# Kernel tuning notes

Measured on AMD Instinct MI355X. Metric: run time of the kernel, lower is better.

## Reference

```python
import jax, jax.numpy as jnp
import numpy as np

B, Q, C = 16, 3000, 1203


def setup_inputs() -> dict:
    key = jax.random.key(0)
    k1, k2, k3, k4 = jax.random.split(key, 4)
    pred_logits = jax.random.normal(k1, (B, Q, C), dtype=jnp.float32)
    pred_boxes = jax.random.uniform(k2, (B, Q, 4), dtype=jnp.float32)
    target_sizes = jax.random.randint(k3, (B, 2), 0, 1333, dtype=jnp.int64)
    class_present = jax.random.randint(k4, (B, C), 0, 2) > 0  # bool [B, C]
    return {
        "pred_logits": pred_logits,
        "pred_boxes": pred_boxes,
        "target_sizes": target_sizes,
        "class_present": class_present,
    }


def reference(pred_logits, pred_boxes, target_sizes, class_present):
    # prob[b,q,c] = sigmoid(logits); keep if prob >= 0.5 * max_q prob[b,:,c]
    # AND class c is in targets[b]['labels'] (class_present mask).
    del target_sizes  # only shape-asserted in the original forward
    prob = jax.nn.sigmoid(pred_logits)                      # [B,Q,C]
    top = jnp.max(prob, axis=1, keepdims=True)              # [B,1,C]
    keep = (prob >= 0.5 * top) & class_present[:, None, :]   # [B,Q,C] bool
    scores = jnp.where(keep, prob, jnp.zeros((), prob.dtype))  # masked scores
    box_keep = jnp.any(keep, axis=2)                        # [B,Q] query kept for some class
    boxes = pred_boxes * box_keep[..., None].astype(pred_boxes.dtype)  # [B,Q,4]
    return scores, keep, boxes
```

## Files before the change

kernel.cpp:

```cpp
#include <hip/hip_runtime.h>
#include <math.h>

#define NB 16
#define NQR 3000
#define NC 1203

typedef float f32x4 __attribute__((ext_vector_type(4)));

__device__ __forceinline__ int lane_proc(float x, float t,
                                         float* __restrict__ s,
                                         float* __restrict__ k) {
    float pf = __builtin_amdgcn_rcpf(1.0f + __expf(-x));
    bool kp;
    float sc;
    if (pf > t + 1e-5f) {
        kp = true;  sc = pf;
    } else if (pf < t - 1e-5f) {
        kp = false; sc = 0.0f;
    } else {
        float e32 = (float)exp(-(double)x);
        float p32 = 1.0f / (1.0f + e32);
        kp = (p32 >= t);
        sc = kp ? p32 : 0.0f;
    }
    *s = sc;
    *k = kp ? 1.0f : 0.0f;
    return kp ? 1 : 0;
}

__global__ void k_partial_max(const float* __restrict__ logits,
                              float* __restrict__ partial,
                              int qc) {
    int c = blockIdx.x * blockDim.x + threadIdx.x;
    int b = blockIdx.y;
    int z = blockIdx.z;
    if (c >= NC) return;
    int q0 = z * qc;
    int q1 = min(NQR, q0 + qc);
    float m = -INFINITY;
    const float* p = logits + ((size_t)(b * NQR + q0)) * NC + c;
    int q = q0;
    for (; q + 8 <= q1; q += 8) {
        float a0 = p[0];
        float a1 = p[NC];
        float a2 = p[2 * NC];
        float a3 = p[3 * NC];
        float a4 = p[4 * NC];
        float a5 = p[5 * NC];
        float a6 = p[6 * NC];
        float a7 = p[7 * NC];
        float m01 = fmaxf(a0, a1), m23 = fmaxf(a2, a3);
        float m45 = fmaxf(a4, a5), m67 = fmaxf(a6, a7);
        m = fmaxf(m, fmaxf(fmaxf(m01, m23), fmaxf(m45, m67)));
        p += 8 * NC;
    }
    for (; q < q1; ++q) {
        m = fmaxf(m, *p);
        p += NC;
    }
    partial[((size_t)z * NB + b) * NC + c] = m;
}

__global__ void k_thresh(const float* __restrict__ partial,
                         const int* __restrict__ cls_present,
                         float* __restrict__ thrf,
                         int nz) {
    int c = blockIdx.x * blockDim.x + threadIdx.x;
    int b = blockIdx.y;
    if (c >= NC) return;
    float m = -INFINITY;
    for (int z = 0; z < nz; ++z)
        m = fmaxf(m, partial[((size_t)z * NB + b) * NC + c]);
    float t;
    if (cls_present[b * NC + c]) {
        float e32  = (float)exp(-(double)m);
        float ptop = 1.0f / (1.0f + e32);
        t = 0.5f * ptop;
    } else {
        t = INFINITY;
    }
    thrf[(size_t)b * NC + c] = t;
}

__global__ __launch_bounds__(256) void k_main(const float* __restrict__ logits,
                                              const float* __restrict__ boxes,
                                              const float* __restrict__ thrf,
                                              float* __restrict__ scores,
                                              float* __restrict__ keep,
                                              float* __restrict__ boxes_out) {
    int wid  = threadIdx.x >> 6;
    int lane = threadIdx.x & 63;
    int row  = blockIdx.x * 4 + wid;
    int b    = row / NQR;

    const float* lrow = logits + (size_t)row * NC;
    const float* tf   = thrf + (size_t)b * NC;
    float* srow = scores + (size_t)row * NC;
    float* krow = keep + (size_t)row * NC;

    int head = row & 3;
    int any = 0;
    float sv, kv;

    f32x4 x[5];
    int cb[5];
    bool act[5];
#pragma unroll
    for (int i = 0; i < 5; ++i) {
        int v = lane + 64 * i;
        act[i] = (v < 300);
        cb[i] = head + 4 * v;
        if (act[i]) x[i] = *(const f32x4*)(lrow + cb[i]);
    }

    if (lane < head) {
        int c = lane;
        any |= lane_proc(lrow[c], tf[c], &sv, &kv);
        __builtin_nontemporal_store(sv, srow + c);
        __builtin_nontemporal_store(kv, krow + c);
    }

#pragma unroll
    for (int i = 0; i < 5; ++i) {
        if (act[i]) {
            int c = cb[i];
            f32x4 x4 = x[i];
            f32x4 s4, k4;
            float s0, s1, s2, s3, k0, k1, k2, k3;
            any |= lane_proc(x4.x, tf[c + 0], &s0, &k0);
            any |= lane_proc(x4.y, tf[c + 1], &s1, &k1);
            any |= lane_proc(x4.z, tf[c + 2], &s2, &k2);
            any |= lane_proc(x4.w, tf[c + 3], &s3, &k3);
            s4 = (f32x4){s0, s1, s2, s3};
            k4 = (f32x4){k0, k1, k2, k3};
            __builtin_nontemporal_store(s4, (f32x4*)(srow + c));
            __builtin_nontemporal_store(k4, (f32x4*)(krow + c));
        }
    }

    if (lane < 3 - head) {
        int c = head + 1200 + lane;
        any |= lane_proc(lrow[c], tf[c], &sv, &kv);
        __builtin_nontemporal_store(sv, srow + c);
        __builtin_nontemporal_store(kv, krow + c);
    }

    unsigned long long m = __ballot(any);
    if (lane == 0) {
        float mm = m ? 1.0f : 0.0f;
        f32x4 bx = *(const f32x4*)(boxes + (size_t)row * 4);
        f32x4 o = bx * mm;
        *(f32x4*)(boxes_out + (size_t)row * 4) = o;
    }
}

extern "C" void kernel_launch(void* const* d_in, const int* in_sizes, int n_in,
                              void* d_out, int out_size, void* d_ws, size_t ws_size,
                              hipStream_t stream) {
    const float* logits      = (const float*)d_in[0];
    const float* boxes       = (const float*)d_in[1];
    const int*   cls_present = (const int*)d_in[3];

    float* scores    = (float*)d_out;
    float* keep      = scores + (size_t)NB * NQR * NC;
    float* boxes_out = keep + (size_t)NB * NQR * NC;

    int nz = 25;
    while (nz > 1 && ((size_t)nz + 1) * NB * NC * sizeof(float) > ws_size)
        nz /= 2;
    float* partial = (float*)d_ws;
    float* thrf    = partial + (size_t)nz * NB * NC;
    int qc = (NQR + nz - 1) / nz;

    dim3 gmax((NC + 255) / 256, NB, nz);
    k_partial_max<<<gmax, 256, 0, stream>>>(logits, partial, qc);

    dim3 gthr((NC + 255) / 256, NB);
    k_thresh<<<gthr, 256, 0, stream>>>(partial, cls_present, thrf, nz);

    k_main<<<(NB * NQR) / 4, 256, 0, stream>>>(logits, boxes, thrf,
                                               scores, keep, boxes_out);
}
```

Before: 195.6 us.

## Split batch into chunks so main pass rereads logits from cache

The three-kernel pipeline now runs over three batch chunks (6, 5 and 5 images), so the max pass and the main pass touch a smaller slice of logits back to back. The intent is for that slice to still sit in the large last-level cache when k_main reads it again, instead of coming from HBM. The main kernel also swaps its up-front load of all five vectors for a one-ahead software prefetch, which lowers register pressure. The cost is more kernel launches and smaller grids per launch, which may hurt occupancy and add launch gaps.

```diff
diff --git a/kernel.cpp b/kernel.cpp
--- a/kernel.cpp
+++ b/kernel.cpp
@@ -30,9 +30,9 @@
 
 __global__ void k_partial_max(const float* __restrict__ logits,
                               float* __restrict__ partial,
-                              int qc) {
+                              int qc, int b0) {
     int c = blockIdx.x * blockDim.x + threadIdx.x;
-    int b = blockIdx.y;
+    int b = blockIdx.y + b0;
     int z = blockIdx.z;
     if (c >= NC) return;
     int q0 = z * qc;
@@ -64,9 +64,9 @@
 __global__ void k_thresh(const float* __restrict__ partial,
                          const int* __restrict__ cls_present,
                          float* __restrict__ thrf,
-                         int nz) {
+                         int nz, int b0) {
     int c = blockIdx.x * blockDim.x + threadIdx.x;
-    int b = blockIdx.y;
+    int b = blockIdx.y + b0;
     if (c >= NC) return;
     float m = -INFINITY;
     for (int z = 0; z < nz; ++z)
@@ -87,10 +87,11 @@
                                               const float* __restrict__ thrf,
                                               float* __restrict__ scores,
                                               float* __restrict__ keep,
-                                              float* __restrict__ boxes_out) {
+                                              float* __restrict__ boxes_out,
+                                              int row0) {
     int wid  = threadIdx.x >> 6;
     int lane = threadIdx.x & 63;
-    int row  = blockIdx.x * 4 + wid;
+    int row  = row0 + blockIdx.x * 4 + wid;
     int b    = row / NQR;
 
     const float* lrow = logits + (size_t)row * NC;
@@ -102,17 +103,6 @@
     int any = 0;
     float sv, kv;
 
-    f32x4 x[5];
-    int cb[5];
-    bool act[5];
-#pragma unroll
-    for (int i = 0; i < 5; ++i) {
-        int v = lane + 64 * i;
-        act[i] = (v < 300);
-        cb[i] = head + 4 * v;
-        if (act[i]) x[i] = *(const f32x4*)(lrow + cb[i]);
-    }
-
     if (lane < head) {
         int c = lane;
         any |= lane_proc(lrow[c], tf[c], &sv, &kv);
@@ -120,22 +110,28 @@
         __builtin_nontemporal_store(kv, krow + c);
     }
 
+    f32x4 cur = *(const f32x4*)(lrow + head + 4 * lane);
 #pragma unroll
     for (int i = 0; i < 5; ++i) {
-        if (act[i]) {
-            int c = cb[i];
-            f32x4 x4 = x[i];
+        int vn = lane + 64 * (i + 1);
+        f32x4 nxt;
+        if (i < 4 && vn < 300)
+            nxt = *(const f32x4*)(lrow + head + 4 * vn);
+        int v = lane + 64 * i;
+        if (v < 300) {
+            int c = head + 4 * v;
             f32x4 s4, k4;
             float s0, s1, s2, s3, k0, k1, k2, k3;
-            any |= lane_proc(x4.x, tf[c + 0], &s0, &k0);
-            any |= lane_proc(x4.y, tf[c + 1], &s1, &k1);
-            any |= lane_proc(x4.z, tf[c + 2], &s2, &k2);
-            any |= lane_proc(x4.w, tf[c + 3], &s3, &k3);
+            any |= lane_proc(cur.x, tf[c + 0], &s0, &k0);
+            any |= lane_proc(cur.y, tf[c + 1], &s1, &k1);
+            any |= lane_proc(cur.z, tf[c + 2], &s2, &k2);
+            any |= lane_proc(cur.w, tf[c + 3], &s3, &k3);
             s4 = (f32x4){s0, s1, s2, s3};
             k4 = (f32x4){k0, k1, k2, k3};
             __builtin_nontemporal_store(s4, (f32x4*)(srow + c));
             __builtin_nontemporal_store(k4, (f32x4*)(krow + c));
         }
+        cur = nxt;
     }
 
     if (lane < 3 - head) {
@@ -172,12 +168,19 @@
     float* thrf    = partial + (size_t)nz * NB * NC;
     int qc = (NQR + nz - 1) / nz;
 
-    dim3 gmax((NC + 255) / 256, NB, nz);
-    k_partial_max<<<gmax, 256, 0, stream>>>(logits, partial, qc);
+    const int bsplit[4] = {0, 6, 11, 16};
+    for (int ch = 0; ch < 3; ++ch) {
+        int b0 = bsplit[ch];
+        int nb = bsplit[ch + 1] - b0;
 
-    dim3 gthr((NC + 255) / 256, NB);
-    k_thresh<<<gthr, 256, 0, stream>>>(partial, cls_present, thrf, nz);
+        dim3 gmax(5, nb, nz);
+        k_partial_max<<<gmax, 256, 0, stream>>>(logits, partial, qc, b0);
 
-    k_main<<<(NB * NQR) / 4, 256, 0, stream>>>(logits, boxes, thrf,
-                                               scores, keep, boxes_out);
+        dim3 gthr(5, nb);
+        k_thresh<<<gthr, 256, 0, stream>>>(partial, cls_present, thrf, nz, b0);
+
+        k_main<<<nb * NQR / 4, 256, 0, stream>>>(logits, boxes, thrf,
+                                                 scores, keep, boxes_out,
+                                                 b0 * NQR);
+    }
 }
```

New measurement: 218.6 us. 11.8% more time.
